# Kernel tuning notes

Measured on AMD Instinct MI355X. Metric: run time of the kernel, lower is better.

Reference implementation:

```python
import jax, jax.numpy as jnp
import numpy as np

NH = 16
NKV = 4
ROPE_BASE = 10000.0
ROPE_TSL = 1024
EPS = 1.1920928955078125e-07  # torch fp32 finfo eps (F.rms_norm default)


def _rms_norm(t):
    return t * jax.lax.rsqrt(jnp.mean(t * t, axis=-1, keepdims=True) + EPS)


def _rope_tables(T, hd):
    # Rotary with rd = hd (rope_dims=0 -> full-head rope). NTK rescale if T > tsl.
    rd = hd
    if T > ROPE_TSL:
        base = ROPE_BASE * (T / ROPE_TSL) ** (rd / (rd - 2))
    else:
        base = ROPE_BASE
    inv_freq = 1.0 / base ** (np.arange(0, rd, 2, dtype=np.float32) / rd)
    t = np.arange(T, dtype=np.float32)
    fr = np.outer(t, inv_freq)  # [T, hd//2]
    return jnp.asarray(np.cos(fr)), jnp.asarray(np.sin(fr))


def _apply_rope(x, cos, sin):
    # x: [B,T,H,D]; cos/sin: [T, D//2] broadcast over batch & heads
    h = x.shape[-1] // 2
    x1, x2 = x[..., :h], x[..., h:]
    c = cos[None, :, None, :]
    s = sin[None, :, None, :]
    return jnp.concatenate((x1 * c + x2 * s, -x1 * s + x2 * c), axis=-1)


def setup_inputs() -> dict:
    key = jax.random.key(0)
    k1, k2, k3, k4, k5 = jax.random.split(key, 5)
    B, T, dim = 2, 2048, 2048
    hd = dim // NH
    kd = NKV * hd
    std = 0.02
    return {
        "x": jax.random.normal(k1, (B, T, dim), dtype=jnp.float32),
        "Wq": jax.random.normal(k2, (dim, dim), dtype=jnp.float32) * std,
        "Wk": jax.random.normal(k3, (kd, dim), dtype=jnp.float32) * std,
        "Wv": jax.random.normal(k4, (kd, dim), dtype=jnp.float32) * std,
        "Wp": jax.random.normal(k5, (dim, dim), dtype=jnp.float32) * std,
        "q_gain": jnp.full((NH,), 1.5, dtype=jnp.float32),
    }


def reference(x, Wq, Wk, Wv, Wp, q_gain):
    B, T, d = x.shape
    hd = d // NH
    g = NH // NKV
    q = (x @ Wq.T).reshape(B, T, NH, hd)
    k = (x @ Wk.T).reshape(B, T, NKV, hd)
    v = (x @ Wv.T).reshape(B, T, NKV, hd)
    q = _rms_norm(q)
    k = _rms_norm(k)
    cos, sin = _rope_tables(T, hd)
    q = _apply_rope(q, cos, sin)
    k = _apply_rope(k, cos, sin)
    q = q * q_gain[None, None, :, None]
    # GQA causal SDPA: group queries per kv head
    qg = q.reshape(B, T, NKV, g, hd)
    scores = jnp.einsum("btkgd,bskd->bkgts", qg, k) / jnp.sqrt(jnp.asarray(hd, x.dtype))
    causal = jnp.tril(jnp.ones((T, T), dtype=bool))
    scores = jnp.where(causal[None, None, None, :, :], scores, jnp.asarray(-jnp.inf, scores.dtype))
    attn = jax.nn.softmax(scores, axis=-1)
    y = jnp.einsum("bkgts,bskd->btkgd", attn, v).reshape(B, T, d)
    return y @ Wp.T
```

## Files before the change

### kernel.cpp

```cpp
#include <hip/hip_runtime.h>
#include <math.h>

#define NH 16
#define NKV 4
#define HD 128
#define DIM 2048
#define GQ 4
#define EPS 1.1920928955078125e-07f

typedef unsigned short u16;
using bf16x8 = __attribute__((ext_vector_type(8))) short;
using f16x4  = __attribute__((ext_vector_type(4))) _Float16;
using f16x8  = __attribute__((ext_vector_type(8))) _Float16;
using f32x4  = __attribute__((ext_vector_type(4))) float;

__device__ inline float fast_exp2(float x) { return __builtin_amdgcn_exp2f(x); }

__device__ inline short f2bf(float f) {
    unsigned u = __builtin_bit_cast(unsigned, f);
    return (short)((u + 0x7FFFu + ((u >> 16) & 1u)) >> 16);
}
__device__ inline u16 f2h(float f) {
    _Float16 h = (_Float16)f;
    return __builtin_bit_cast(u16, h);
}

#define ASYNC_LOAD16(g, l)                                                        \
    __builtin_amdgcn_global_load_lds(                                             \
        (const __attribute__((address_space(1))) unsigned*)(g),                   \
        (__attribute__((address_space(3))) unsigned*)(l), 16, 0, 0)

__global__ __launch_bounds__(256) void cvt_bf16(const float* __restrict__ src,
                                                u16* __restrict__ dst, int n4) {
    int i = blockIdx.x * 256 + threadIdx.x;
    if (i < n4) {
        float4 f = ((const float4*)src)[i];
        ushort4 o;
        o.x = (u16)f2bf(f.x); o.y = (u16)f2bf(f.y);
        o.z = (u16)f2bf(f.z); o.w = (u16)f2bf(f.w);
        ((ushort4*)dst)[i] = o;
    }
}

__global__ __launch_bounds__(64) void rope_tab(float* __restrict__ ct,
                                               float* __restrict__ st,
                                               double base) {
    const int t = blockIdx.x;
    const int j = threadIdx.x;
    const float inv_freq = (float)pow(base, -(double)j / 64.0);
    const float fr = (float)t * inv_freq;
    ct[t * 64 + j] = cosf(fr);
    st[t * 64 + j] = sinf(fr);
}

#define GTK 32

__global__ __launch_bounds__(256) void gemm_bf16(const u16* __restrict__ A,
                                                 const u16* __restrict__ W,
                                                 float* __restrict__ C,
                                                 int M, int N, int K) {
    __shared__ u16 As[128 * GTK];
    __shared__ u16 Bs[128 * GTK];
    const int tid = threadIdx.x;
    const int wave = tid >> 6;
    const int lane = tid & 63;
    const int l16 = lane & 15;
    const int quad = lane >> 4;
    const int wm = wave >> 1;
    const int wn = wave & 1;
    const int m0 = blockIdx.x * 128;
    const int n0 = blockIdx.y * 128;

    const int srow = lane >> 2;
    const int scol = (lane & 3) * 8;

    f32x4 acc[4][4];
#pragma unroll
    for (int i = 0; i < 4; i++)
#pragma unroll
        for (int j = 0; j < 4; j++) acc[i][j] = (f32x4){0.f, 0.f, 0.f, 0.f};

    for (int k0 = 0; k0 < K; k0 += GTK) {
        __syncthreads();
#pragma unroll
        for (int j = 0; j < 2; j++) {
            const int rb = wave * 32 + j * 16;
            const u16* ga = A + (size_t)(m0 + rb + srow) * K + k0 + scol;
            const u16* gb = W + (size_t)(n0 + rb + srow) * K + k0 + scol;
            ASYNC_LOAD16(ga, &As[rb * GTK]);
            ASYNC_LOAD16(gb, &Bs[rb * GTK]);
        }
        __syncthreads();

        bf16x8 af[4], bfr[4];
#pragma unroll
        for (int mt = 0; mt < 4; mt++)
            af[mt] = *(const bf16x8*)&As[(wm * 64 + mt * 16 + l16) * GTK + quad * 8];
#pragma unroll
        for (int nt = 0; nt < 4; nt++)
            bfr[nt] = *(const bf16x8*)&Bs[(wn * 64 + nt * 16 + l16) * GTK + quad * 8];
#pragma unroll
        for (int mt = 0; mt < 4; mt++)
#pragma unroll
            for (int nt = 0; nt < 4; nt++)
                acc[mt][nt] = __builtin_amdgcn_mfma_f32_16x16x32_bf16(
                    af[mt], bfr[nt], acc[mt][nt], 0, 0, 0);
    }

#pragma unroll
    for (int mt = 0; mt < 4; mt++)
#pragma unroll
        for (int nt = 0; nt < 4; nt++)
#pragma unroll
            for (int r = 0; r < 4; r++)
                C[(size_t)(m0 + wm * 64 + mt * 16 + quad * 4 + r) * N +
                  n0 + wn * 64 + nt * 16 + l16] = acc[mt][nt][r];
}

__global__ __launch_bounds__(256) void gemm_qkv(const u16* __restrict__ A,
                                                const u16* __restrict__ W,
                                                u16* __restrict__ q16,
                                                u16* __restrict__ k16,
                                                u16* __restrict__ vt16,
                                                const float* __restrict__ ctab,
                                                const float* __restrict__ stab,
                                                const float* __restrict__ q_gain,
                                                int T) {
    __shared__ u16 As[128 * GTK];
    __shared__ u16 Bs[128 * GTK];
    const int tid = threadIdx.x;
    const int wave = tid >> 6;
    const int lane = tid & 63;
    const int l16 = lane & 15;
    const int quad = lane >> 4;
    const int m0 = blockIdx.x * 128;
    const int n0 = blockIdx.y * 128;
    const int K = DIM;

    const int srow = lane >> 2;
    const int scol = (lane & 3) * 8;

    f32x4 acc[2][8];
#pragma unroll
    for (int i = 0; i < 2; i++)
#pragma unroll
        for (int j = 0; j < 8; j++) acc[i][j] = (f32x4){0.f, 0.f, 0.f, 0.f};

    for (int k0 = 0; k0 < K; k0 += GTK) {
        __syncthreads();
#pragma unroll
        for (int j = 0; j < 2; j++) {
            const int rb = wave * 32 + j * 16;
            const u16* ga = A + (size_t)(m0 + rb + srow) * K + k0 + scol;
            const u16* gb = W + (size_t)(n0 + rb + srow) * K + k0 + scol;
            ASYNC_LOAD16(ga, &As[rb * GTK]);
            ASYNC_LOAD16(gb, &Bs[rb * GTK]);
        }
        __syncthreads();

        bf16x8 af[2], bfr[8];
#pragma unroll
        for (int mt = 0; mt < 2; mt++)
            af[mt] = *(const bf16x8*)&As[(wave * 32 + mt * 16 + l16) * GTK + quad * 8];
#pragma unroll
        for (int nt = 0; nt < 8; nt++)
            bfr[nt] = *(const bf16x8*)&Bs[(nt * 16 + l16) * GTK + quad * 8];
#pragma unroll
        for (int mt = 0; mt < 2; mt++)
#pragma unroll
            for (int nt = 0; nt < 8; nt++)
                acc[mt][nt] = __builtin_amdgcn_mfma_f32_16x16x32_bf16(
                    af[mt], bfr[nt], acc[mt][nt], 0, 0, 0);
    }

    if (n0 < 2048 + 512) {
        const bool isQ = (n0 < 2048);
        const float gval = isQ ? (q_gain[n0 >> 7] * 0.08838834764831843f * 1.4426950408889634f)
                               : 1.0f;
        float ss[2][4];
#pragma unroll
        for (int mt = 0; mt < 2; mt++)
#pragma unroll
            for (int r = 0; r < 4; r++) {
                float s = 0.f;
#pragma unroll
                for (int nt = 0; nt < 8; nt++) {
                    float a = acc[mt][nt][r];
                    s = fmaf(a, a, s);
                }
                s += __shfl_xor(s, 1);
                s += __shfl_xor(s, 2);
                s += __shfl_xor(s, 4);
                s += __shfl_xor(s, 8);
                ss[mt][r] = s;
            }
#pragma unroll
        for (int mt = 0; mt < 2; mt++)
#pragma unroll
            for (int r = 0; r < 4; r++) {
                const float scale = rsqrtf(ss[mt][r] * (1.0f / HD) + EPS) * gval;
                const int m = m0 + wave * 32 + mt * 16 + quad * 4 + r;
                const int t = m & (T - 1);
                const float* ct = ctab + t * 64;
                const float* st = stab + t * 64;
                u16* dst = isQ ? (q16 + (size_t)m * 2048 + n0)
                               : (k16 + (size_t)m * 512 + (n0 - 2048));
#pragma unroll
                for (int nt = 0; nt < 4; nt++) {
                    const int j = nt * 16 + l16;
                    const float c = ct[j], s = st[j];
                    const float x1 = acc[mt][nt][r] * scale;
                    const float x2 = acc[mt][nt + 4][r] * scale;
                    dst[j]      = (u16)f2bf(x1 * c + x2 * s);
                    dst[j + 64] = (u16)f2bf(x2 * c - x1 * s);
                }
            }
    } else {
        const int kvh = (n0 - 2560) >> 7;
#pragma unroll
        for (int mt = 0; mt < 2; mt++) {
            const int mb = m0 + wave * 32 + mt * 16 + quad * 4;
            const int b = mb / 2048;
            const int t0 = mb & (T - 1);
#pragma unroll
            for (int nt = 0; nt < 8; nt++) {
                const int d = nt * 16 + l16;
                ushort4 o;
                o.x = f2h(acc[mt][nt][0]);
                o.y = f2h(acc[mt][nt][1]);
                o.z = f2h(acc[mt][nt][2]);
                o.w = f2h(acc[mt][nt][3]);
                *(ushort4*)(vt16 + ((size_t)((b * NKV + kvh) * HD + d)) * T + t0) = o;
            }
        }
    }
}

#define QT 64
#define SK 64
#define KP 136
#define VPP 72

__global__ __launch_bounds__(256) void flash3(const u16* __restrict__ q16,
                                              const u16* __restrict__ k16,
                                              const u16* __restrict__ vt16,
                                              u16* __restrict__ y16, int T) {
    __shared__ u16 Ks[2][SK * KP];
    __shared__ u16 Vt[2][HD * VPP];

    const int tid = threadIdx.x;
    const int wave = tid >> 6;
    const int lane = tid & 63;
    const int l16 = lane & 15;
    const int quad = lane >> 4;

    const int bid = blockIdx.x;
    const int bh = bid & 31;
    const int pr = bid >> 5;
    const int h = bh & 15;
    const int b = bh >> 4;
    const int kv = h / GQ;

    const u16* kg = k16 + ((size_t)b * T * NKV + kv) * HD;
    const u16* vg = vt16 + (size_t)(b * NKV + kv) * HD * T;

    int kr[4], kc_[4], vd[4], vch[4];
#pragma unroll
    for (int j = 0; j < 4; j++) {
        const int idx = tid + j * 256;
        kr[j] = idx >> 4; kc_[j] = (idx & 15) * 8;
        vd[j] = idx >> 3; vch[j] = idx & 7;
    }

    int4 kpre[4], vpre[4];

#pragma unroll
    for (int half = 0; half < 2; half++) {
        const int qt = half ? (T / QT - 1 - pr) : pr;
        const int q0 = qt * QT;
        const int qglob = q0 + wave * 16 + l16;
        const int nts = q0 / SK + 1;

        bf16x8 qf[4];
        {
            const u16* qp = q16 + ((size_t)(b * T + qglob) * NH + h) * HD;
#pragma unroll
            for (int kc = 0; kc < 4; kc++)
                qf[kc] = *(const bf16x8*)(qp + kc * 32 + quad * 8);
        }

        f32x4 of[8];
#pragma unroll
        for (int i = 0; i < 8; i++) of[i] = (f32x4){0.f, 0.f, 0.f, 0.f};
        float m_i = -1e30f, l_i = 0.0f;

#pragma unroll
        for (int j = 0; j < 4; j++)
            kpre[j] = *(const int4*)(kg + (size_t)kr[j] * (NKV * HD) + kc_[j]);
#pragma unroll
        for (int j = 0; j < 4; j++)
            vpre[j] = *(const int4*)(vg + (size_t)vd[j] * T + vch[j] * 8);

        for (int it = 0; it < nts; it++) {
            const int cur = it & 1;
            __syncthreads();
#pragma unroll
            for (int j = 0; j < 4; j++)
                *(int4*)&Ks[cur][kr[j] * KP + kc_[j]] = kpre[j];
#pragma unroll
            for (int j = 0; j < 4; j++) {
                const int ch = vch[j];
                u16* row = &Vt[cur][vd[j] * VPP];
                const int p1 = ((2 * ch) & 3) * 16 + (ch >> 1) * 4;
                const int p2 = ((2 * ch + 1) & 3) * 16 + (ch >> 1) * 4;
                *(int2*)&row[p1] = make_int2(vpre[j].x, vpre[j].y);
                *(int2*)&row[p2] = make_int2(vpre[j].z, vpre[j].w);
            }
            __syncthreads();

            if (it + 1 < nts) {
                const int s1 = (it + 1) * SK;
#pragma unroll
                for (int j = 0; j < 4; j++)
                    kpre[j] = *(const int4*)(kg + (size_t)(s1 + kr[j]) * (NKV * HD) + kc_[j]);
#pragma unroll
                for (int j = 0; j < 4; j++)
                    vpre[j] = *(const int4*)(vg + (size_t)vd[j] * T + s1 + vch[j] * 8);
            }

            f32x4 sf[4];
#pragma unroll
            for (int st = 0; st < 4; st++) sf[st] = (f32x4){0.f, 0.f, 0.f, 0.f};
#pragma unroll
            for (int kc = 0; kc < 4; kc++)
#pragma unroll
                for (int st = 0; st < 4; st++) {
                    bf16x8 kf = *(const bf16x8*)&Ks[cur][(st * 16 + l16) * KP + kc * 32 + quad * 8];
                    sf[st] = __builtin_amdgcn_mfma_f32_16x16x32_bf16(kf, qf[kc], sf[st], 0, 0, 0);
                }

            if (it == nts - 1) {
#pragma unroll
                for (int st = 0; st < 4; st++)
#pragma unroll
                    for (int r = 0; r < 4; r++)
                        if (q0 + st * 16 + quad * 4 + r > qglob) sf[st][r] = -1e30f;
            }

            float tm = -1e30f;
#pragma unroll
            for (int st = 0; st < 4; st++)
#pragma unroll
                for (int r = 0; r < 4; r++) tm = fmaxf(tm, sf[st][r]);
            tm = fmaxf(tm, __shfl_xor(tm, 16));
            tm = fmaxf(tm, __shfl_xor(tm, 32));

            const float mprev = m_i;
            const float mnew = fmaxf(mprev, tm);
            m_i = mnew;
            const float alpha = fast_exp2(mprev - mnew);

            f16x4 pf[4];
            float ls = 0.0f;
#pragma unroll
            for (int st = 0; st < 4; st++)
#pragma unroll
                for (int r = 0; r < 4; r++) {
                    float e = fast_exp2(sf[st][r] - mnew);
                    ls += e;
                    pf[st][r] = (_Float16)e;
                }
            ls += __shfl_xor(ls, 16);
            ls += __shfl_xor(ls, 32);
            l_i = alpha * l_i + ls;

            if (__ballot(mnew > mprev)) {
#pragma unroll
                for (int dt = 0; dt < 8; dt++)
#pragma unroll
                    for (int r = 0; r < 4; r++) of[dt][r] *= alpha;
            }

#pragma unroll
            for (int st2 = 0; st2 < 2; st2++)
#pragma unroll
                for (int dt = 0; dt < 8; dt++) {
                    f16x8 v8 = *(const f16x8*)&Vt[cur][(dt * 16 + l16) * VPP + quad * 16 + st2 * 8];
                    f16x4 va = {v8[0], v8[1], v8[2], v8[3]};
                    f16x4 vb = {v8[4], v8[5], v8[6], v8[7]};
                    of[dt] = __builtin_amdgcn_mfma_f32_16x16x16f16(va, pf[st2 * 2], of[dt], 0, 0, 0);
                    of[dt] = __builtin_amdgcn_mfma_f32_16x16x16f16(vb, pf[st2 * 2 + 1], of[dt], 0, 0, 0);
                }
        }

        const float inv = 1.0f / l_i;
        u16* yp = y16 + ((size_t)(b * T + qglob) * NH + h) * HD + quad * 4;
#pragma unroll
        for (int dt = 0; dt < 8; dt++) {
            ushort4 o;
            o.x = (u16)f2bf(of[dt][0] * inv);
            o.y = (u16)f2bf(of[dt][1] * inv);
            o.z = (u16)f2bf(of[dt][2] * inv);
            o.w = (u16)f2bf(of[dt][3] * inv);
            *(ushort4*)(yp + dt * 16) = o;
        }
    }
}

extern "C" void kernel_launch(void* const* d_in, const int* in_sizes, int n_in,
                              void* d_out, int out_size, void* d_ws, size_t ws_size,
                              hipStream_t stream) {
    const float* x      = (const float*)d_in[0];
    const float* Wq     = (const float*)d_in[1];
    const float* Wk     = (const float*)d_in[2];
    const float* Wv     = (const float*)d_in[3];
    const float* Wp     = (const float*)d_in[4];
    const float* q_gain = (const float*)d_in[5];
    float* out = (float*)d_out;

    const int B = 2;
    const int BT = in_sizes[0] / DIM;
    const int T = BT / B;
    const int KD = NKV * HD;

    u16* x16   = (u16*)d_ws;
    u16* wqkv  = x16 + (size_t)BT * DIM;
    u16* wp16  = wqkv + (size_t)3072 * DIM;
    u16* q16   = wp16 + (size_t)DIM * DIM;
    u16* k16   = q16 + (size_t)BT * DIM;
    u16* vt16  = k16 + (size_t)BT * KD;
    float* ctab = (float*)(vt16 + (size_t)BT * KD);
    float* stab = ctab + (size_t)T * 64;
    u16* y16   = x16;

    double base = 10000.0;
    if (T > 1024) base = 10000.0 * pow((double)T / 1024.0, 128.0 / 126.0);

    const int nx4  = BT * DIM / 4;
    const int nwq4 = DIM * DIM / 4;
    const int nwk4 = KD * DIM / 4;

    cvt_bf16<<<(nx4 + 255) / 256, 256, 0, stream>>>(x, x16, nx4);
    cvt_bf16<<<(nwq4 + 255) / 256, 256, 0, stream>>>(Wq, wqkv, nwq4);
    cvt_bf16<<<(nwk4 + 255) / 256, 256, 0, stream>>>(Wk, wqkv + (size_t)2048 * DIM, nwk4);
    cvt_bf16<<<(nwk4 + 255) / 256, 256, 0, stream>>>(Wv, wqkv + (size_t)2560 * DIM, nwk4);
    cvt_bf16<<<(nwq4 + 255) / 256, 256, 0, stream>>>(Wp, wp16, nwq4);
    rope_tab<<<T, 64, 0, stream>>>(ctab, stab, base);

    gemm_qkv<<<dim3(BT / 128, 3072 / 128), 256, 0, stream>>>(
        x16, wqkv, q16, k16, vt16, ctab, stab, q_gain, T);

    flash3<<<32 * (T / QT / 2), 256, 0, stream>>>(q16, k16, vt16, y16, T);

    gemm_bf16<<<dim3(BT / 128, DIM / 128), 256, 0, stream>>>(y16, wp16, out, BT, DIM, DIM);
}
```

Before: 377.3 us.

## Use async global-to-LDS loads with XOR-swizzled K/V tiles in flash attention

The attention kernel no longer stages the next K and V tiles through registers and then writes them to padded shared memory. Each wave instead issues direct global-to-LDS async loads into the other buffer, and bank conflicts are avoided with an XOR swizzle of 16-byte chunks rather than row padding. This removes one barrier per iteration and the register pressure of the prefetch buffers, and lets the copy overlap with the MFMA work. The V reads now fetch 4-element fragments per MFMA instead of 8-element loads split in two. Correctness depends on the barrier waiting for the async loads to complete.

```diff
diff --git a/kernel.cpp b/kernel.cpp
--- a/kernel.cpp
+++ b/kernel.cpp
@@ -11,7 +11,6 @@
 typedef unsigned short u16;
 using bf16x8 = __attribute__((ext_vector_type(8))) short;
 using f16x4  = __attribute__((ext_vector_type(4))) _Float16;
-using f16x8  = __attribute__((ext_vector_type(8))) _Float16;
 using f32x4  = __attribute__((ext_vector_type(4))) float;
 
 __device__ inline float fast_exp2(float x) { return __builtin_amdgcn_exp2f(x); }
@@ -238,15 +237,13 @@
 
 #define QT 64
 #define SK 64
-#define KP 136
-#define VPP 72
-
-__global__ __launch_bounds__(256) void flash3(const u16* __restrict__ q16,
+
+__global__ __launch_bounds__(256) void flash4(const u16* __restrict__ q16,
                                               const u16* __restrict__ k16,
                                               const u16* __restrict__ vt16,
                                               u16* __restrict__ y16, int T) {
-    __shared__ u16 Ks[2][SK * KP];
-    __shared__ u16 Vt[2][HD * VPP];
+    __shared__ u16 Ks[2][SK * 128];
+    __shared__ u16 Vt[2][HD * 64];
 
     const int tid = threadIdx.x;
     const int wave = tid >> 6;
@@ -264,17 +261,12 @@
     const u16* kg = k16 + ((size_t)b * T * NKV + kv) * HD;
     const u16* vg = vt16 + (size_t)(b * NKV + kv) * HD * T;
 
-    int kr[4], kc_[4], vd[4], vch[4];
-#pragma unroll
-    for (int j = 0; j < 4; j++) {
-        const int idx = tid + j * 256;
-        kr[j] = idx >> 4; kc_[j] = (idx & 15) * 8;
-        vd[j] = idx >> 3; vch[j] = idx & 7;
-    }
-
-    int4 kpre[4], vpre[4];
-
-#pragma unroll
+    const int krow_in_seg = lane >> 4;
+    const int kclog_base = lane & 15;
+    const int vrow_in_seg = lane >> 3;
+    const int vclog = (lane & 7) ^ (lane >> 3);
+
+#pragma unroll 1
     for (int half = 0; half < 2; half++) {
         const int qt = half ? (T / QT - 1 - pr) : pr;
         const int q0 = qt * QT;
@@ -294,38 +286,34 @@
         for (int i = 0; i < 8; i++) of[i] = (f32x4){0.f, 0.f, 0.f, 0.f};
         float m_i = -1e30f, l_i = 0.0f;
 
-#pragma unroll
-        for (int j = 0; j < 4; j++)
-            kpre[j] = *(const int4*)(kg + (size_t)kr[j] * (NKV * HD) + kc_[j]);
-#pragma unroll
-        for (int j = 0; j < 4; j++)
-            vpre[j] = *(const int4*)(vg + (size_t)vd[j] * T + vch[j] * 8);
+        __syncthreads();
+#pragma unroll
+        for (int j = 0; j < 4; j++) {
+            const int seg = wave * 4 + j;
+            const int r = seg * 4 + krow_in_seg;
+            const int clog = kclog_base ^ (r & 15);
+            ASYNC_LOAD16(kg + (size_t)r * (NKV * HD) + clog * 8, &Ks[0][seg * 512]);
+            const int d = seg * 8 + vrow_in_seg;
+            ASYNC_LOAD16(vg + (size_t)d * T + vclog * 8, &Vt[0][seg * 512]);
+        }
 
         for (int it = 0; it < nts; it++) {
             const int cur = it & 1;
             __syncthreads();
-#pragma unroll
-            for (int j = 0; j < 4; j++)
-                *(int4*)&Ks[cur][kr[j] * KP + kc_[j]] = kpre[j];
-#pragma unroll
-            for (int j = 0; j < 4; j++) {
-                const int ch = vch[j];
-                u16* row = &Vt[cur][vd[j] * VPP];
-                const int p1 = ((2 * ch) & 3) * 16 + (ch >> 1) * 4;
-                const int p2 = ((2 * ch + 1) & 3) * 16 + (ch >> 1) * 4;
-                *(int2*)&row[p1] = make_int2(vpre[j].x, vpre[j].y);
-                *(int2*)&row[p2] = make_int2(vpre[j].z, vpre[j].w);
-            }
-            __syncthreads();
 
             if (it + 1 < nts) {
                 const int s1 = (it + 1) * SK;
 #pragma unroll
-                for (int j = 0; j < 4; j++)
-                    kpre[j] = *(const int4*)(kg + (size_t)(s1 + kr[j]) * (NKV * HD) + kc_[j]);
-#pragma unroll
-                for (int j = 0; j < 4; j++)
-                    vpre[j] = *(const int4*)(vg + (size_t)vd[j] * T + s1 + vch[j] * 8);
+                for (int j = 0; j < 4; j++) {
+                    const int seg = wave * 4 + j;
+                    const int r = seg * 4 + krow_in_seg;
+                    const int clog = kclog_base ^ (r & 15);
+                    ASYNC_LOAD16(kg + (size_t)(s1 + r) * (NKV * HD) + clog * 8,
+                                 &Ks[cur ^ 1][seg * 512]);
+                    const int d = seg * 8 + vrow_in_seg;
+                    ASYNC_LOAD16(vg + (size_t)d * T + s1 + vclog * 8,
+                                 &Vt[cur ^ 1][seg * 512]);
+                }
             }
 
             f32x4 sf[4];
@@ -335,7 +323,9 @@
             for (int kc = 0; kc < 4; kc++)
 #pragma unroll
                 for (int st = 0; st < 4; st++) {
-                    bf16x8 kf = *(const bf16x8*)&Ks[cur][(st * 16 + l16) * KP + kc * 32 + quad * 8];
+                    const int row = st * 16 + l16;
+                    bf16x8 kf = *(const bf16x8*)
+                        &Ks[cur][row * 128 + (((kc * 4 + quad) ^ l16) * 8)];
                     sf[st] = __builtin_amdgcn_mfma_f32_16x16x32_bf16(kf, qf[kc], sf[st], 0, 0, 0);
                 }
 
@@ -382,15 +372,17 @@
             }
 
 #pragma unroll
-            for (int st2 = 0; st2 < 2; st2++)
+            for (int st = 0; st < 4; st++) {
+                const int clog = st * 2 + (quad >> 1);
 #pragma unroll
                 for (int dt = 0; dt < 8; dt++) {
-                    f16x8 v8 = *(const f16x8*)&Vt[cur][(dt * 16 + l16) * VPP + quad * 16 + st2 * 8];
-                    f16x4 va = {v8[0], v8[1], v8[2], v8[3]};
-                    f16x4 vb = {v8[4], v8[5], v8[6], v8[7]};
-                    of[dt] = __builtin_amdgcn_mfma_f32_16x16x16f16(va, pf[st2 * 2], of[dt], 0, 0, 0);
-                    of[dt] = __builtin_amdgcn_mfma_f32_16x16x16f16(vb, pf[st2 * 2 + 1], of[dt], 0, 0, 0);
-                }
+                    const int d = dt * 16 + l16;
+                    const int phys = clog ^ (l16 & 7);
+                    f16x4 va = *(const f16x4*)
+                        &Vt[cur][d * 64 + phys * 8 + (quad & 1) * 4];
+                    of[dt] = __builtin_amdgcn_mfma_f32_16x16x16f16(va, pf[st], of[dt], 0, 0, 0);
+                }
+            }
         }
 
         const float inv = 1.0f / l_i;
@@ -450,7 +442,7 @@
     gemm_qkv<<<dim3(BT / 128, 3072 / 128), 256, 0, stream>>>(
         x16, wqkv, q16, k16, vt16, ctab, stab, q_gain, T);
 
-    flash3<<<32 * (T / QT / 2), 256, 0, stream>>>(q16, k16, vt16, y16, T);
+    flash4<<<32 * (T / QT / 2), 256, 0, stream>>>(q16, k16, vt16, y16, T);
 
     gemm_bf16<<<dim3(BT / 128, DIM / 128), 256, 0, stream>>>(y16, wp16, out, BT, DIM, DIM);
 }
```

Result: faster. 336.6 us (-10.8%).
